# Kernel tuning notes

Measured on AMD Instinct MI355X. Metric: run time of the kernel, lower is better.

## Reference

```python
import jax, jax.numpy as jnp
import numpy as np

N = 50000     # nodes
E = 400000    # nnz per hop matrix
K1 = 4        # K + 1 hops (K = 3)
D = 1280      # in_dim (pad_features target_dim)
H = 256       # hidden_dim


def setup_inputs() -> dict:
    key = jax.random.key(0)
    k0, k1, k2, k3, k4, k5 = jax.random.split(key, 6)
    X = jax.random.normal(k0, (N, D), dtype=jnp.float32)
    rows = jax.random.randint(k1, (K1, E), 0, N, dtype=jnp.int32)
    cols = jax.random.randint(k2, (K1, E), 0, N, dtype=jnp.int32)
    vals = jax.random.uniform(k3, (K1, E), dtype=jnp.float32)
    W = jax.random.normal(k4, (K1, D, H), dtype=jnp.float32) * 0.02
    b = jax.random.normal(k5, (K1, H), dtype=jnp.float32) * 0.02
    alpha = jnp.ones((1,), dtype=jnp.float32) * 0.25  # PReLU default init
    return {"X": X, "rows": rows, "cols": cols, "vals": vals,
            "W": W, "b": b, "alpha": alpha}


def _spmm(rows_k, cols_k, vals_k, X):
    # sparse A_k @ X: gather source rows, scale by edge values, scatter-add to dest rows
    return jax.ops.segment_sum(vals_k[:, None] * X[cols_k], rows_k, num_segments=N)


def reference(X, rows, cols, vals, W, b, alpha):
    out = jnp.zeros((N, H), dtype=X.dtype)
    for k in range(K1):  # small fixed hop count, structurally distinct matrices
        tmp = _spmm(rows[k], cols[k], vals[k], X)       # [N, D]
        out = out + tmp @ W[k] + b[k]                    # [N, H]
    # PReLU with single shared alpha
    return jnp.where(out >= 0, out, alpha * out)
```

## Files before the change

kernel.cpp:

```cpp
#include <hip/hip_runtime.h>
#include <hip/hip_bf16.h>
#include <stdint.h>

#define N_NODES 50000
#define E_EDGES 400000
#define K1H 4
#define D_IN 1280
#define H_OUT 256
#define NTOT 1024
#define MP 50176
#define NFULL 704
#define NHALF 160
#define HALF_BASE 45056
#define CAP 128

#define NB_BSUM 1
#define NB_SCAT 6250
#define NB_CVTW 5120
#define NB_CVTX 62720

typedef float f32x4 __attribute__((ext_vector_type(4)));
typedef short s16x8 __attribute__((ext_vector_type(8)));

#define GLOBAL_AS __attribute__((address_space(1)))
#define LDS_AS __attribute__((address_space(3)))

__device__ __forceinline__ void g2lds16(const void* g, void* l) {
    __builtin_amdgcn_global_load_lds((const GLOBAL_AS uint32_t*)g,
                                     (LDS_AS uint32_t*)l, 16, 0, 0);
}

__device__ __forceinline__ ushort f2bf(float x) {
    uint32_t u = __float_as_uint(x);
    uint32_t r = u + 0x7FFFu + ((u >> 16) & 1u);
    return (ushort)(r >> 16);
}
__device__ __forceinline__ float bf2f(ushort u) {
    return __uint_as_float(((uint32_t)u) << 16);
}

__global__ void __launch_bounds__(256)
prep_kernel(const float* __restrict__ X, ushort* __restrict__ Xb,
            const float* __restrict__ W, ushort* __restrict__ WbT,
            const int* __restrict__ rows, const int* __restrict__ cols,
            const float* __restrict__ vals, int* __restrict__ cnt,
            int2* __restrict__ edges, const float* __restrict__ b,
            float* __restrict__ bsum) {
    const int blk = blockIdx.x, tid = threadIdx.x;
    if (blk == 0) {
        bsum[tid] = b[tid] + b[256 + tid] + b[512 + tid] + b[768 + tid];
    } else if (blk < NB_BSUM + NB_SCAT) {
        const int i = (blk - NB_BSUM) * 256 + tid;
        const int k = i / E_EDGES;
        const int r = rows[i];
        const int pos = atomicAdd(&cnt[r], 1);
        if (pos < CAP)
            edges[(size_t)r * CAP + pos] =
                make_int2((cols[i] << 10) | (k << 8), __float_as_int(vals[i]));
    } else if (blk < NB_BSUM + NB_SCAT + NB_CVTW) {
        const int o = (blk - NB_BSUM - NB_SCAT) * 256 + tid;
        const int n = o / D_IN, d = o - n * D_IN;
        const int k = n >> 8, h = n & 255;
        WbT[o] = f2bf(W[(k * D_IN + d) * H_OUT + h]);
    } else {
        const int i = ((blk - NB_BSUM - NB_SCAT - NB_CVTW) * 256 + tid) * 4;
        ushort4 o4;
        if (i < N_NODES * D_IN) {
            const float4 v = *(const float4*)(X + i);
            o4.x = f2bf(v.x); o4.y = f2bf(v.y); o4.z = f2bf(v.z); o4.w = f2bf(v.w);
        } else {
            o4.x = 0; o4.y = 0; o4.z = 0; o4.w = 0;
        }
        *(ushort4*)(Xb + i) = o4;
    }
}

#define BARR() __builtin_amdgcn_s_barrier()
#define LGKM0() { asm volatile("s_waitcnt lgkmcnt(0)" ::: "memory"); \
                  __builtin_amdgcn_sched_barrier(0); }

template<int N> __device__ __forceinline__ void vmc() {
    if constexpr (N == 0)      asm volatile("s_waitcnt vmcnt(0)" ::: "memory");
    else if constexpr (N == 3) asm volatile("s_waitcnt vmcnt(3)" ::: "memory");
    else if constexpr (N == 4) asm volatile("s_waitcnt vmcnt(4)" ::: "memory");
    else if constexpr (N == 6) asm volatile("s_waitcnt vmcnt(6)" ::: "memory");
    else if constexpr (N == 8) asm volatile("s_waitcnt vmcnt(8)" ::: "memory");
    else static_assert(N == 0, "unsupported vmcnt");
}

#define lA(BUF) (lds0 + ((BUF) * 2 + 0) * 16384)
#define lB(BUF) (lds0 + ((BUF) * 2 + 1) * 16384)

#define STAGE_A(BUF, G, KT) { \
    if constexpr (MTF == 4) { \
        _Pragma("unroll") for (int r = 0; r < 2; ++r) \
            g2lds16(pA + ((r) * 128 + (G) * 64) * D_IN + (KT) * 64, \
                    lA(BUF) + (t + (G) * 512 + (r) * 1024) * 8); \
    } else { \
        const int r64 = t >> 3, hi = (t >> 8) & 1; \
        g2lds16(pA + ((G) * 32 + hi * 32) * D_IN + (KT) * 64, \
                lA(BUF) + (((G) * 32 + (r64 & 31) + hi * 64) * 8 + (t & 7)) * 8); \
    } }
#define STAGE_B(BUF, G, KT) { _Pragma("unroll") \
    for (int r = 0; r < 2; ++r) \
        g2lds16(pB + ((r) * 128 + (G) * 32) * D_IN + (KT) * 64, \
                lB(BUF) + (t + wm * 256 + (G) * 256 + (r) * 1024) * 8); }
#define LDA_F(BUF, MH) { _Pragma("unroll") \
    for (int mt = 0; mt < MTF; ++mt) { \
        const int m = wm * (MTF * 32) + (MH) * (MTF * 16) + mt * 16 + l16; \
        _Pragma("unroll") for (int ks = 0; ks < 2; ++ks) \
            af[mt][ks] = *(const s16x8*)(lA(BUF) + (m * 8 + ((ks * 4 + quad) ^ (l16 & 7))) * 8); } }
#define LDB_F(BUF, NH) { _Pragma("unroll") \
    for (int nt = 0; nt < 2; ++nt) { \
        const int n = wn * 64 + (NH) * 32 + nt * 16 + l16; \
        _Pragma("unroll") for (int ks = 0; ks < 2; ++ks) \
            bfr[NH][nt][ks] = *(const s16x8*)(lB(BUF) + (n * 8 + ((ks * 4 + quad) ^ (l16 & 7))) * 8); } }
#define MMA_Q(MH, NH) { __builtin_amdgcn_s_setprio(1); \
    _Pragma("unroll") for (int mt = 0; mt < MTF; ++mt) \
        _Pragma("unroll") for (int nt = 0; nt < 2; ++nt) \
            _Pragma("unroll") for (int ks = 0; ks < 2; ++ks) \
                acc[(MH) * MTF + mt][(NH) * 2 + nt] = \
                    __builtin_amdgcn_mfma_f32_16x16x32_bf16(af[mt][ks], bfr[NH][nt][ks], \
                        acc[(MH) * MTF + mt][(NH) * 2 + nt], 0, 0, 0); \
    __builtin_amdgcn_s_setprio(0); }

template<int MTF>
__device__ __forceinline__ void gemm_body(ushort* lds0,
        const ushort* __restrict__ Xb, const ushort* __restrict__ WbT,
        ushort* __restrict__ Yb, const int rowBase, const int colBase, const int t) {
    constexpr int AL = MTF / 2;
    constexpr int VA = 2 * AL + 2;
    constexpr int VB = 2 * AL + 4;
    constexpr int VT = AL + 2;

    const int w = t >> 6, lane = t & 63;
    const int quad = lane >> 4, l16 = lane & 15;
    const int wm = w >> 2, wn = w & 3;

    f32x4 acc[MTF * 2][4] = {};
    s16x8 af[MTF][2];
    s16x8 bfr[2][2][2];

    const int kcg = (t & 7) ^ ((t >> 3) & 7);
    const ushort* pA = Xb + (rowBase + (t >> 3)) * D_IN + kcg * 8;
    const ushort* pB = WbT + (colBase + (t >> 3) + wm * 32) * D_IN + kcg * 8;

    STAGE_A(0, 0, 0); STAGE_B(0, 0, 0); STAGE_A(0, 1, 0); STAGE_B(0, 1, 0);
    STAGE_A(1, 0, 1); STAGE_B(1, 0, 1);
    vmc<VB>();
    BARR();

#pragma unroll 1
    for (int i = 0; i < 9; ++i) {
        const int kt0 = 2 * i;
        LDA_F(0, 0); LDB_F(0, 0); STAGE_A(1, 1, kt0 + 1); vmc<VA>();
        BARR(); LGKM0(); MMA_Q(0, 0);
        LDB_F(0, 1); STAGE_B(1, 1, kt0 + 1);
        BARR(); LGKM0(); MMA_Q(0, 1);
        LDA_F(0, 1); STAGE_A(0, 0, kt0 + 2);
        BARR(); LGKM0(); MMA_Q(1, 0);
        STAGE_B(0, 0, kt0 + 2); vmc<VB>();
        BARR(); MMA_Q(1, 1);
        LDA_F(1, 0); LDB_F(1, 0); STAGE_A(0, 1, kt0 + 2); vmc<VA>();
        BARR(); LGKM0(); MMA_Q(0, 0);
        LDB_F(1, 1); STAGE_B(0, 1, kt0 + 2);
        BARR(); LGKM0(); MMA_Q(0, 1);
        LDA_F(1, 1); STAGE_A(1, 0, kt0 + 3);
        BARR(); LGKM0(); MMA_Q(1, 0);
        STAGE_B(1, 0, kt0 + 3); vmc<VB>();
        BARR(); MMA_Q(1, 1);
    }

    LDA_F(0, 0); LDB_F(0, 0); STAGE_A(1, 1, 19); vmc<VA>();
    BARR(); LGKM0(); MMA_Q(0, 0);
    LDB_F(0, 1); STAGE_B(1, 1, 19);
    BARR(); LGKM0(); MMA_Q(0, 1);
    LDA_F(0, 1);
    BARR(); LGKM0(); MMA_Q(1, 0);
    vmc<VT>();
    BARR(); MMA_Q(1, 1);
    LDA_F(1, 0); LDB_F(1, 0); vmc<0>();
    BARR(); LGKM0(); MMA_Q(0, 0);
    LDB_F(1, 1);
    BARR(); LGKM0(); MMA_Q(0, 1);
    LDA_F(1, 1);
    BARR(); LGKM0(); MMA_Q(1, 0);
    MMA_Q(1, 1);

    #pragma unroll
    for (int mh = 0; mh < 2; ++mh)
      #pragma unroll
      for (int mt = 0; mt < MTF; ++mt)
        #pragma unroll
        for (int nh = 0; nh < 2; ++nh)
          #pragma unroll
          for (int nt = 0; nt < 2; ++nt) {
            const int rr = rowBase + wm * (MTF * 32) + mh * (MTF * 16) + mt * 16 + quad * 4;
            const int cc = colBase + wn * 64 + nh * 32 + nt * 16 + l16;
            #pragma unroll
            for (int r = 0; r < 4; ++r)
                Yb[(rr + r) * NTOT + cc] = f2bf(acc[mh * MTF + mt][nh * 2 + nt][r]);
          }
}

__global__ void __launch_bounds__(512, 2)
gemm_kernel(const ushort* __restrict__ Xb, const ushort* __restrict__ WbT,
            ushort* __restrict__ Yb) {
    __shared__ ushort lds[2][2][256 * 64];
    const int bid = blockIdx.x;
    const int t = threadIdx.x;
    if (bid < NFULL) {
        const int xcd = bid & 7, j = bid >> 3;
        const int j2 = xcd * 88 + j;
        gemm_body<4>(&lds[0][0][0], Xb, WbT, Yb, (j2 >> 2) * 256, (j2 & 3) * 256, t);
    } else {
        const int hb = bid - NFULL;
        const int j2 = (hb & 7) * 20 + (hb >> 3);
        gemm_body<2>(&lds[0][0][0], Xb, WbT, Yb,
                     HALF_BASE + (j2 >> 2) * 128, (j2 & 3) * 256, t);
    }
}

#undef STAGE_A
#undef STAGE_B
#undef LDA_F
#undef LDB_F
#undef MMA_Q
#undef lA
#undef lB

__global__ void __launch_bounds__(256)
spmm_kernel(const int2* __restrict__ edges, const int* __restrict__ cnt,
            const ushort* __restrict__ Yb, const float* __restrict__ bsum,
            const float* __restrict__ alpha, float* __restrict__ out) {
    const int wid = threadIdx.x >> 6, lane = threadIdx.x & 63;
    const int row = blockIdx.x * 4 + wid;
    const int h0 = lane * 4;

    const float4 bb = *(const float4*)(bsum + h0);
    float4 acc = bb;

    const int2* eb = edges + (size_t)row * CAP;
    int e = cnt[row]; if (e > CAP) e = CAP;
    int j = 0;
    for (; j + 8 <= e; j += 8) {
        int2 er[8]; ushort4 y[8]; float v[8];
        #pragma unroll
        for (int s = 0; s < 8; ++s) er[s] = eb[j + s];
        #pragma unroll
        for (int s = 0; s < 8; ++s) y[s] = *(const ushort4*)(Yb + er[s].x + h0);
        #pragma unroll
        for (int s = 0; s < 8; ++s) v[s] = __int_as_float(er[s].y);
        #pragma unroll
        for (int s = 0; s < 8; ++s) {
            acc.x += v[s] * bf2f(y[s].x);
            acc.y += v[s] * bf2f(y[s].y);
            acc.z += v[s] * bf2f(y[s].z);
            acc.w += v[s] * bf2f(y[s].w);
        }
    }
    for (; j < e; ++j) {
        const int2 ed = eb[j];
        const float v = __int_as_float(ed.y);
        const ushort4 y = *(const ushort4*)(Yb + ed.x + h0);
        acc.x += v * bf2f(y.x);
        acc.y += v * bf2f(y.y);
        acc.z += v * bf2f(y.z);
        acc.w += v * bf2f(y.w);
    }

    const float a = alpha[0];
    float4 o;
    o.x = acc.x >= 0.f ? acc.x : a * acc.x;
    o.y = acc.y >= 0.f ? acc.y : a * acc.y;
    o.z = acc.z >= 0.f ? acc.z : a * acc.z;
    o.w = acc.w >= 0.f ? acc.w : a * acc.w;
    *(float4*)(out + row * H_OUT + h0) = o;
}

static inline size_t align256(size_t x) { return (x + 255) & ~(size_t)255; }

extern "C" void kernel_launch(void* const* d_in, const int* in_sizes, int n_in,
                              void* d_out, int out_size, void* d_ws, size_t ws_size,
                              hipStream_t stream) {
    const float* X     = (const float*)d_in[0];
    const int*   rows  = (const int*)d_in[1];
    const int*   cols  = (const int*)d_in[2];
    const float* vals  = (const float*)d_in[3];
    const float* W     = (const float*)d_in[4];
    const float* b     = (const float*)d_in[5];
    const float* alpha = (const float*)d_in[6];
    float* out = (float*)d_out;

    char* ws = (char*)d_ws;
    size_t off = 0;
    ushort* Xb  = (ushort*)(ws + off); off = align256(off + (size_t)MP * D_IN * 2);
    ushort* WbT = (ushort*)(ws + off); off = align256(off + (size_t)NTOT * D_IN * 2);
    ushort* Yb  = (ushort*)(ws + off); off = align256(off + (size_t)MP * NTOT * 2);
    int* cnt    = (int*)(ws + off);    off = align256(off + (size_t)N_NODES * 4);
    int2* edges = (int2*)(ws + off);   off = align256(off + (size_t)N_NODES * CAP * 8);
    float* bsum = (float*)(ws + off);  off = align256(off + (size_t)H_OUT * 4);

    hipMemsetAsync(cnt, 0, (size_t)N_NODES * 4, stream);

    prep_kernel<<<NB_BSUM + NB_SCAT + NB_CVTW + NB_CVTX, 256, 0, stream>>>(
        X, Xb, W, WbT, rows, cols, vals, cnt, edges, b, bsum);
    gemm_kernel<<<NFULL + NHALF, 512, 0, stream>>>(Xb, WbT, Yb);
    spmm_kernel<<<N_NODES / 4, 256, 0, stream>>>(edges, cnt, Yb, bsum, alpha, out);
}
```

Measured before the change: 728.6 us.

## Replace fixed-capacity edge buckets with CSR built by histogram, scan and placement

Per-row edge buckets of fixed capacity 128 are replaced by a compact CSR layout. It is built in three steps: an atomic histogram of rows, a single-block prefix scan, and an atomic placement pass. The SpMM kernel then reads edges through base offsets. This removes the large sparse bucket array and the capacity cap, which could silently drop edges, and gives denser edge reads. In exchange it adds three kernel launches, one of them a serial single-block scan, and reads the rows array twice.

```diff
diff --git a/kernel.cpp b/kernel.cpp
--- a/kernel.cpp
+++ b/kernel.cpp
@@ -5,6 +5,7 @@
 #define N_NODES 50000
 #define E_EDGES 400000
 #define K1H 4
+#define NEDGE 1600000
 #define D_IN 1280
 #define H_OUT 256
 #define NTOT 1024
@@ -12,10 +13,8 @@
 #define NFULL 704
 #define NHALF 160
 #define HALF_BASE 45056
-#define CAP 128
 
 #define NB_BSUM 1
-#define NB_SCAT 6250
 #define NB_CVTW 5120
 #define NB_CVTX 62720
 
@@ -39,31 +38,68 @@
     return __uint_as_float(((uint32_t)u) << 16);
 }
 
+
+__global__ void __launch_bounds__(256)
+hist_kernel(const int* __restrict__ rows, int* __restrict__ cnt) {
+    const int i = blockIdx.x * 256 + threadIdx.x;
+    atomicAdd(&cnt[rows[i]], 1);
+}
+
+__global__ void __launch_bounds__(1024)
+scan_kernel(const int* __restrict__ cnt, int* __restrict__ base,
+            int* __restrict__ cur) {
+    __shared__ int lds[1024];
+    const int tid = threadIdx.x;
+    const int i0 = tid * 49;
+    int s = 0;
+    for (int j = 0; j < 49; ++j) {
+        const int i = i0 + j;
+        s += (i < N_NODES) ? cnt[i] : 0;
+    }
+    lds[tid] = s;
+    __syncthreads();
+    for (int d = 1; d < 1024; d <<= 1) {
+        const int add = (tid >= d) ? lds[tid - d] : 0;
+        __syncthreads();
+        lds[tid] += add;
+        __syncthreads();
+    }
+    int run = (tid > 0) ? lds[tid - 1] : 0;
+    for (int j = 0; j < 49; ++j) {
+        const int i = i0 + j;
+        if (i < N_NODES) {
+            base[i] = run;
+            cur[i] = run;
+            run += cnt[i];
+        }
+    }
+}
+
+__global__ void __launch_bounds__(256)
+place_kernel(const int* __restrict__ rows, const int* __restrict__ cols,
+             const float* __restrict__ vals, int* __restrict__ cur,
+             int2* __restrict__ edges) {
+    const int i = blockIdx.x * 256 + threadIdx.x;
+    const int k = i / E_EDGES;
+    const int r = rows[i];
+    const int pos = atomicAdd(&cur[r], 1);
+    edges[pos] = make_int2((cols[i] << 10) | (k << 8), __float_as_int(vals[i]));
+}
+
 __global__ void __launch_bounds__(256)
 prep_kernel(const float* __restrict__ X, ushort* __restrict__ Xb,
             const float* __restrict__ W, ushort* __restrict__ WbT,
-            const int* __restrict__ rows, const int* __restrict__ cols,
-            const float* __restrict__ vals, int* __restrict__ cnt,
-            int2* __restrict__ edges, const float* __restrict__ b,
-            float* __restrict__ bsum) {
+            const float* __restrict__ b, float* __restrict__ bsum) {
     const int blk = blockIdx.x, tid = threadIdx.x;
     if (blk == 0) {
         bsum[tid] = b[tid] + b[256 + tid] + b[512 + tid] + b[768 + tid];
-    } else if (blk < NB_BSUM + NB_SCAT) {
-        const int i = (blk - NB_BSUM) * 256 + tid;
-        const int k = i / E_EDGES;
-        const int r = rows[i];
-        const int pos = atomicAdd(&cnt[r], 1);
-        if (pos < CAP)
-            edges[(size_t)r * CAP + pos] =
-                make_int2((cols[i] << 10) | (k << 8), __float_as_int(vals[i]));
-    } else if (blk < NB_BSUM + NB_SCAT + NB_CVTW) {
-        const int o = (blk - NB_BSUM - NB_SCAT) * 256 + tid;
+    } else if (blk < NB_BSUM + NB_CVTW) {
+        const int o = (blk - NB_BSUM) * 256 + tid;
         const int n = o / D_IN, d = o - n * D_IN;
         const int k = n >> 8, h = n & 255;
         WbT[o] = f2bf(W[(k * D_IN + d) * H_OUT + h]);
     } else {
-        const int i = ((blk - NB_BSUM - NB_SCAT - NB_CVTW) * 256 + tid) * 4;
+        const int i = ((blk - NB_BSUM - NB_CVTW) * 256 + tid) * 4;
         ushort4 o4;
         if (i < N_NODES * D_IN) {
             const float4 v = *(const float4*)(X + i);
@@ -230,9 +266,10 @@
 #undef lB
 
 __global__ void __launch_bounds__(256)
-spmm_kernel(const int2* __restrict__ edges, const int* __restrict__ cnt,
-            const ushort* __restrict__ Yb, const float* __restrict__ bsum,
-            const float* __restrict__ alpha, float* __restrict__ out) {
+spmm_kernel(const int2* __restrict__ edges, const int* __restrict__ base,
+            const int* __restrict__ cnt, const ushort* __restrict__ Yb,
+            const float* __restrict__ bsum, const float* __restrict__ alpha,
+            float* __restrict__ out) {
     const int wid = threadIdx.x >> 6, lane = threadIdx.x & 63;
     const int row = blockIdx.x * 4 + wid;
     const int h0 = lane * 4;
@@ -240,8 +277,8 @@
     const float4 bb = *(const float4*)(bsum + h0);
     float4 acc = bb;
 
-    const int2* eb = edges + (size_t)row * CAP;
-    int e = cnt[row]; if (e > CAP) e = CAP;
+    const int2* eb = edges + base[row];
+    const int e = cnt[row];
     int j = 0;
     for (; j + 8 <= e; j += 8) {
         int2 er[8]; ushort4 y[8]; float v[8];
@@ -298,13 +335,18 @@
     ushort* WbT = (ushort*)(ws + off); off = align256(off + (size_t)NTOT * D_IN * 2);
     ushort* Yb  = (ushort*)(ws + off); off = align256(off + (size_t)MP * NTOT * 2);
     int* cnt    = (int*)(ws + off);    off = align256(off + (size_t)N_NODES * 4);
-    int2* edges = (int2*)(ws + off);   off = align256(off + (size_t)N_NODES * CAP * 8);
+    int* base   = (int*)(ws + off);    off = align256(off + (size_t)N_NODES * 4);
+    int* cur    = (int*)(ws + off);    off = align256(off + (size_t)N_NODES * 4);
+    int2* edges = (int2*)(ws + off);   off = align256(off + (size_t)NEDGE * 8);
     float* bsum = (float*)(ws + off);  off = align256(off + (size_t)H_OUT * 4);
 
     hipMemsetAsync(cnt, 0, (size_t)N_NODES * 4, stream);
 
-    prep_kernel<<<NB_BSUM + NB_SCAT + NB_CVTW + NB_CVTX, 256, 0, stream>>>(
-        X, Xb, W, WbT, rows, cols, vals, cnt, edges, b, bsum);
+    hist_kernel<<<NEDGE / 256, 256, 0, stream>>>(rows, cnt);
+    scan_kernel<<<1, 1024, 0, stream>>>(cnt, base, cur);
+    place_kernel<<<NEDGE / 256, 256, 0, stream>>>(rows, cols, vals, cur, edges);
+    prep_kernel<<<NB_BSUM + NB_CVTW + NB_CVTX, 256, 0, stream>>>(
+        X, Xb, W, WbT, b, bsum);
     gemm_kernel<<<NFULL + NHALF, 512, 0, stream>>>(Xb, WbT, Yb);
-    spmm_kernel<<<N_NODES / 4, 256, 0, stream>>>(edges, cnt, Yb, bsum, alpha, out);
-}
+    spmm_kernel<<<N_NODES / 4, 256, 0, stream>>>(edges, base, cnt, Yb, bsum, alpha, out);
+}
```

After: 914.0 us. +25.4%, slower.

## Overlap edge bucketing scatter with GEMM using extra waves in GEMM blocks

Applied to the files above, without the earlier changes.

Removes the edge-bucketing (atomic scatter into per-row edge lists) from the prep kernel and runs it in two extra wavefronts added to each GEMM block, so the scatter runs while the bf16 GEMM executes. The extra waves each handle a contiguous slice of edges, then issue a fixed count of barriers to stay in step with the GEMM waves' barriers before returning. This hides the atomic-heavy scatter behind matrix work. It raises the block to 640 threads, which may tighten the per-wave register budget, and the hard-coded barrier count has to match the GEMM body exactly.

```diff
diff --git a/kernel.cpp b/kernel.cpp
--- a/kernel.cpp
+++ b/kernel.cpp
@@ -5,6 +5,7 @@
 #define N_NODES 50000
 #define E_EDGES 400000
 #define K1H 4
+#define NEDGE 1600000
 #define D_IN 1280
 #define H_OUT 256
 #define NTOT 1024
@@ -13,9 +14,9 @@
 #define NHALF 160
 #define HALF_BASE 45056
 #define CAP 128
+#define EPB 1852
 
 #define NB_BSUM 1
-#define NB_SCAT 6250
 #define NB_CVTW 5120
 #define NB_CVTX 62720
 
@@ -42,28 +43,17 @@
 __global__ void __launch_bounds__(256)
 prep_kernel(const float* __restrict__ X, ushort* __restrict__ Xb,
             const float* __restrict__ W, ushort* __restrict__ WbT,
-            const int* __restrict__ rows, const int* __restrict__ cols,
-            const float* __restrict__ vals, int* __restrict__ cnt,
-            int2* __restrict__ edges, const float* __restrict__ b,
-            float* __restrict__ bsum) {
+            const float* __restrict__ b, float* __restrict__ bsum) {
     const int blk = blockIdx.x, tid = threadIdx.x;
     if (blk == 0) {
         bsum[tid] = b[tid] + b[256 + tid] + b[512 + tid] + b[768 + tid];
-    } else if (blk < NB_BSUM + NB_SCAT) {
-        const int i = (blk - NB_BSUM) * 256 + tid;
-        const int k = i / E_EDGES;
-        const int r = rows[i];
-        const int pos = atomicAdd(&cnt[r], 1);
-        if (pos < CAP)
-            edges[(size_t)r * CAP + pos] =
-                make_int2((cols[i] << 10) | (k << 8), __float_as_int(vals[i]));
-    } else if (blk < NB_BSUM + NB_SCAT + NB_CVTW) {
-        const int o = (blk - NB_BSUM - NB_SCAT) * 256 + tid;
+    } else if (blk < NB_BSUM + NB_CVTW) {
+        const int o = (blk - NB_BSUM) * 256 + tid;
         const int n = o / D_IN, d = o - n * D_IN;
         const int k = n >> 8, h = n & 255;
         WbT[o] = f2bf(W[(k * D_IN + d) * H_OUT + h]);
     } else {
-        const int i = ((blk - NB_BSUM - NB_SCAT - NB_CVTW) * 256 + tid) * 4;
+        const int i = ((blk - NB_BSUM - NB_CVTW) * 256 + tid) * 4;
         ushort4 o4;
         if (i < N_NODES * D_IN) {
             const float4 v = *(const float4*)(X + i);
@@ -203,12 +193,36 @@
           }
 }
 
-__global__ void __launch_bounds__(512, 2)
+__global__ void __launch_bounds__(640, 2)
 gemm_kernel(const ushort* __restrict__ Xb, const ushort* __restrict__ WbT,
-            ushort* __restrict__ Yb) {
+            ushort* __restrict__ Yb, const int* __restrict__ rows,
+            const int* __restrict__ cols, const float* __restrict__ vals,
+            int* __restrict__ cnt, int2* __restrict__ edges) {
     __shared__ ushort lds[2][2][256 * 64];
     const int bid = blockIdx.x;
     const int t = threadIdx.x;
+
+    if (t >= 512) {
+        const int td = t - 512;
+        const int e0 = bid * EPB;
+        int eEnd = e0 + EPB; if (eEnd > NEDGE) eEnd = NEDGE;
+        #pragma unroll
+        for (int j = 0; j < 15; ++j) {
+            const int i = e0 + td + 128 * j;
+            if (i < eEnd) {
+                const int r = rows[i];
+                const int k = i / E_EDGES;
+                const int pos = atomicAdd(&cnt[r], 1);
+                if (pos < CAP)
+                    edges[(size_t)r * CAP + pos] =
+                        make_int2((cols[i] << 10) | (k << 8), __float_as_int(vals[i]));
+            }
+        }
+        #pragma unroll 1
+        for (int p = 0; p < 80; ++p) BARR();
+        return;
+    }
+
     if (bid < NFULL) {
         const int xcd = bid & 7, j = bid >> 3;
         const int j2 = xcd * 88 + j;
@@ -303,8 +317,9 @@
 
     hipMemsetAsync(cnt, 0, (size_t)N_NODES * 4, stream);
 
-    prep_kernel<<<NB_BSUM + NB_SCAT + NB_CVTW + NB_CVTX, 256, 0, stream>>>(
-        X, Xb, W, WbT, rows, cols, vals, cnt, edges, b, bsum);
-    gemm_kernel<<<NFULL + NHALF, 512, 0, stream>>>(Xb, WbT, Yb);
+    prep_kernel<<<NB_BSUM + NB_CVTW + NB_CVTX, 256, 0, stream>>>(
+        X, Xb, W, WbT, b, bsum);
+    gemm_kernel<<<NFULL + NHALF, 640, 0, stream>>>(
+        Xb, WbT, Yb, rows, cols, vals, cnt, edges);
     spmm_kernel<<<N_NODES / 4, 256, 0, stream>>>(edges, cnt, Yb, bsum, alpha, out);
 }
```

New measurement: 1.533 ms. +110.3%, slower.
